# Kernel optimization log

Measured on AMD Instinct MI355X. Metric: run time of the kernel, lower is better.

Reference implementation:

```python
import jax, jax.numpy as jnp
import numpy as np

EPS = 1e-6
NUM_GROUPS = 32


def group_norm(x, w, b):
    # x: [B, C, W, H, L]
    B, C = x.shape[0], x.shape[1]
    xr = x.reshape(B, NUM_GROUPS, C // NUM_GROUPS, -1)
    mu = jnp.mean(xr, axis=(2, 3), keepdims=True)
    var = jnp.var(xr, axis=(2, 3), keepdims=True)
    xn = ((xr - mu) * jax.lax.rsqrt(var + EPS)).reshape(x.shape)
    return xn * w[None, :, None, None, None] + b[None, :, None, None, None]


def setup_inputs() -> dict:
    key = jax.random.key(0)
    ks = jax.random.split(key, 8)
    B, C, W, H, L = 2, 512, 16, 16, 16
    s = 1.0 / np.sqrt(C)
    return {
        "x": jax.random.normal(ks[0], (B, C, W, H, L), dtype=jnp.float32),
        "gn_w": jnp.ones((C,), dtype=jnp.float32),
        "gn_b": jnp.zeros((C,), dtype=jnp.float32),
        "q_w": jax.random.normal(ks[1], (C, C), dtype=jnp.float32) * s,
        "q_b": jnp.zeros((C,), dtype=jnp.float32),
        "k_w": jax.random.normal(ks[2], (C, C), dtype=jnp.float32) * s,
        "k_b": jnp.zeros((C,), dtype=jnp.float32),
        "v_w": jax.random.normal(ks[3], (C, C), dtype=jnp.float32) * s,
        "v_b": jnp.zeros((C,), dtype=jnp.float32),
        "p_w": jax.random.normal(ks[4], (C, C), dtype=jnp.float32) * s,
        "p_b": jnp.zeros((C,), dtype=jnp.float32),
    }


def reference(x, gn_w, gn_b, q_w, q_b, k_w, k_b, v_w, v_b, p_w, p_b):
    B, C, W, H, L = x.shape
    h = group_norm(x, gn_w, gn_b)
    hf = h.reshape(B, C, -1)  # [B, C, N]
    # 1x1 Conv3d == channel matmul: out[b,o,n] = sum_c w[o,c] * h[b,c,n] + b[o]
    q = jnp.einsum('oc,bcn->bon', q_w, hf) + q_b[None, :, None]
    k = jnp.einsum('oc,bcn->bon', k_w, hf) + k_b[None, :, None]
    v = jnp.einsum('oc,bcn->bon', v_w, hf) + v_b[None, :, None]
    scale = jnp.asarray(C, x.dtype) ** -0.5
    # w_[b,i,j] = sum_c q[b,c,i] * k[b,c,j]
    w_ = jnp.einsum('bci,bcj->bij', q, k) * scale
    w_ = jax.nn.softmax(w_, axis=2)
    # h_[b,c,i] = sum_j v[b,c,j] * w_[b,i,j]
    attn = jnp.einsum('bcj,bij->bci', v, w_)
    proj = jnp.einsum('oc,bcn->bon', p_w, attn) + p_b[None, :, None]
    return x + proj.reshape(B, C, W, H, L)
```

## Files before the change

### kernel.cpp

```cpp
#include <hip/hip_runtime.h>


typedef __bf16 bf16;
typedef __attribute__((ext_vector_type(8))) __bf16 bf16x8;
typedef __attribute__((ext_vector_type(4))) __bf16 bf16x4;
typedef __attribute__((ext_vector_type(4))) float f32x4;

#define CC 512
#define NN 4096
#define BM 128
#define BN 128
#define BK 64
#define SCALE_L2E 0.06376237870903338f

__device__ __forceinline__ void gload16(const bf16* g, bf16* l) {
    __builtin_amdgcn_global_load_lds(
        (const __attribute__((address_space(1))) unsigned int*)g,
        (__attribute__((address_space(3))) unsigned int*)l, 16, 0, 0);
}

__device__ __forceinline__ void gemm_core(
    const bf16* __restrict__ A, int lda,
    const bf16* __restrict__ B, int ldb,
    int kBeg, int kEnd, int m0, int n0, f32x4 acc[4][4])
{
    __shared__ __align__(16) bf16 Als[2][BM][BK];
    __shared__ __align__(16) bf16 Bls[2][BN][BK];
    const int t    = threadIdx.x;
    const int lane = t & 63;
    const int wid  = t >> 6;
    const int wm   = (wid >> 1) * 64;
    const int wn   = (wid & 1) * 64;
    const int fr   = lane & 15;
    const int kq   = lane >> 4;
    const int r_   = t >> 3;
    const int cbs  = (t & 7) ^ (r_ & 7);
    const int dcol = (t & 7) * 8;
    const int cs0  = ((kq)     ^ (fr & 7)) * 8;
    const int cs1  = ((kq + 4) ^ (fr & 7)) * 8;

    const bf16* Ab = A + (size_t)(m0 + r_) * lda + cbs * 8;
    const bf16* Bb = B + (size_t)(n0 + r_) * ldb + cbs * 8;

#define STAGE_G(bufi, kk) do {                                              \
        _Pragma("unroll")                                                   \
        for (int i = 0; i < 4; ++i)                                         \
            gload16(Ab + (kk) + (size_t)(i * 32) * lda,                     \
                    &Als[bufi][i * 32 + r_][dcol]);                         \
        _Pragma("unroll")                                                   \
        for (int i = 0; i < 4; ++i)                                         \
            gload16(Bb + (kk) + (size_t)(i * 32) * ldb,                     \
                    &Bls[bufi][i * 32 + r_][dcol]);                         \
    } while (0)

    int cur = 0;
    STAGE_G(0, kBeg);
    __syncthreads();
    for (int k0 = kBeg; k0 < kEnd; k0 += BK) {
        if (k0 + BK < kEnd) STAGE_G(cur ^ 1, k0 + BK);
        #pragma unroll
        for (int h = 0; h < 2; ++h) {
            const int cs = h ? cs1 : cs0;
            bf16x8 af[4], bg[4];
            #pragma unroll
            for (int f = 0; f < 4; ++f) {
                af[f] = *(const bf16x8*)&Als[cur][wm + f * 16 + fr][cs];
                bg[f] = *(const bf16x8*)&Bls[cur][wn + f * 16 + fr][cs];
            }
            #pragma unroll
            for (int fm = 0; fm < 4; ++fm)
                #pragma unroll
                for (int fn = 0; fn < 4; ++fn)
                    acc[fm][fn] = __builtin_amdgcn_mfma_f32_16x16x32_bf16(
                        af[fm], bg[fn], acc[fm][fn], 0, 0, 0);
        }
        __syncthreads();
        cur ^= 1;
    }
#undef STAGE_G
}

__device__ __forceinline__ void gemm_core64(
    const bf16* __restrict__ A, int lda,
    const bf16* __restrict__ B, int ldb,
    int kBeg, int kEnd, int m0, int n0, f32x4 acc[2][4])
{
    __shared__ __align__(16) bf16 Als[2][64][BK];
    __shared__ __align__(16) bf16 Bls[2][BN][BK];
    const int t    = threadIdx.x;
    const int lane = t & 63;
    const int wid  = t >> 6;
    const int wm   = (wid >> 1) * 32;
    const int wn   = (wid & 1) * 64;
    const int fr   = lane & 15;
    const int kq   = lane >> 4;
    const int r_   = t >> 3;
    const int cbs  = (t & 7) ^ (r_ & 7);
    const int dcol = (t & 7) * 8;
    const int cs0  = ((kq)     ^ (fr & 7)) * 8;
    const int cs1  = ((kq + 4) ^ (fr & 7)) * 8;

    const bf16* Ab = A + (size_t)(m0 + r_) * lda + cbs * 8;
    const bf16* Bb = B + (size_t)(n0 + r_) * ldb + cbs * 8;

#define STAGE_G64(bufi, kk) do {                                            \
        _Pragma("unroll")                                                   \
        for (int i = 0; i < 2; ++i)                                         \
            gload16(Ab + (kk) + (size_t)(i * 32) * lda,                     \
                    &Als[bufi][i * 32 + r_][dcol]);                         \
        _Pragma("unroll")                                                   \
        for (int i = 0; i < 4; ++i)                                         \
            gload16(Bb + (kk) + (size_t)(i * 32) * ldb,                     \
                    &Bls[bufi][i * 32 + r_][dcol]);                         \
    } while (0)

    int cur = 0;
    STAGE_G64(0, kBeg);
    __syncthreads();
    for (int k0 = kBeg; k0 < kEnd; k0 += BK) {
        if (k0 + BK < kEnd) STAGE_G64(cur ^ 1, k0 + BK);
        #pragma unroll
        for (int h = 0; h < 2; ++h) {
            const int cs = h ? cs1 : cs0;
            bf16x8 af[2], bg[4];
            #pragma unroll
            for (int f = 0; f < 2; ++f)
                af[f] = *(const bf16x8*)&Als[cur][wm + f * 16 + fr][cs];
            #pragma unroll
            for (int f = 0; f < 4; ++f)
                bg[f] = *(const bf16x8*)&Bls[cur][wn + f * 16 + fr][cs];
            #pragma unroll
            for (int fm = 0; fm < 2; ++fm)
                #pragma unroll
                for (int fn = 0; fn < 4; ++fn)
                    acc[fm][fn] = __builtin_amdgcn_mfma_f32_16x16x32_bf16(
                        af[fm], bg[fn], acc[fm][fn], 0, 0, 0);
        }
        __syncthreads();
        cur ^= 1;
    }
#undef STAGE_G64
}

__global__ __launch_bounds__(256) void convert_w_kernel(
    const float* __restrict__ qw, const float* __restrict__ kw,
    const float* __restrict__ pw, bf16* __restrict__ dst)
{
    const int which = blockIdx.y;
    const float* src = which == 0 ? qw : which == 1 ? kw : pw;
    const int slot  = which == 2 ? 3 : which;
    bf16* d = dst + (size_t)slot * (CC * CC);
    const int f4 = blockIdx.x * 256 + threadIdx.x;
    float4 v = ((const float4*)src)[f4];
    bf16x4 o;
    o[0] = (bf16)v.x; o[1] = (bf16)v.y; o[2] = (bf16)v.z; o[3] = (bf16)v.w;
    ((bf16x4*)d)[f4] = o;
}

__global__ __launch_bounds__(256) void vwT_kernel(
    const float* __restrict__ vw, bf16* __restrict__ vwT)
{
    const int k0 = blockIdx.x * 64;
    const int c0 = blockIdx.y * 64;
    const int t  = threadIdx.x;
    const int tk = t & 15, tc = t >> 4;
    float o[4][4];
    #pragma unroll
    for (int j = 0; j < 4; ++j) {
        const int c = c0 + tc * 4 + j;
        float4 v = *(const float4*)(vw + (size_t)c * CC + k0 + tk * 4);
        o[j][0] = v.x; o[j][1] = v.y; o[j][2] = v.z; o[j][3] = v.w;
    }
    #pragma unroll
    for (int i = 0; i < 4; ++i) {
        bf16x4 w4;
        w4[0] = (bf16)o[0][i]; w4[1] = (bf16)o[1][i];
        w4[2] = (bf16)o[2][i]; w4[3] = (bf16)o[3][i];
        *(bf16x4*)(vwT + (size_t)(k0 + tk * 4 + i) * CC + c0 + tc * 4) = w4;
    }
}

__global__ __launch_bounds__(256) void wb_kernel(
    const float* __restrict__ pw, const float* __restrict__ vb,
    float* __restrict__ wb)
{
    const int o = blockIdx.x * 256 + threadIdx.x;
    const float4* row = (const float4*)(pw + (size_t)o * CC);
    const float4* v4  = (const float4*)vb;
    float s = 0.f;
    #pragma unroll 4
    for (int i = 0; i < 128; ++i) {
        float4 a = row[i], b = v4[i];
        s += a.x * b.x + a.y * b.y + a.z * b.z + a.w * b.w;
    }
    wb[o] = s;
}

__global__ __launch_bounds__(256) void gn_stats_kernel(
    const float* __restrict__ x, float* __restrict__ mr)
{
    const int bg = blockIdx.x >> 2;
    const int qq = blockIdx.x & 3;
    const float4* base = (const float4*)(x + (size_t)bg * 16 * NN);
    const int t = threadIdx.x;
    float s = 0.f, sq = 0.f;
    #pragma unroll 4
    for (int i = 0; i < 16; ++i) {
        float4 v = base[(qq * 16 + i) * 256 + t];
        s  += v.x + v.y + v.z + v.w;
        sq += v.x * v.x + v.y * v.y + v.z * v.z + v.w * v.w;
    }
    #pragma unroll
    for (int o = 32; o > 0; o >>= 1) { s += __shfl_xor(s, o); sq += __shfl_xor(sq, o); }
    __shared__ float rs[4], rq[4];
    const int lane = t & 63, wid = t >> 6;
    if (lane == 0) { rs[wid] = s; rq[wid] = sq; }
    __syncthreads();
    if (t == 0) {
        atomicAdd(&mr[bg * 2],     rs[0] + rs[1] + rs[2] + rs[3]);
        atomicAdd(&mr[bg * 2 + 1], rq[0] + rq[1] + rq[2] + rq[3]);
    }
}

__global__ __launch_bounds__(256) void gn_apply_T_kernel(
    const float* __restrict__ x, const float* __restrict__ gw,
    const float* __restrict__ gb, const float* __restrict__ mr,
    bf16* __restrict__ hT)
{
    const int b  = blockIdx.z;
    const int n0 = blockIdx.x * 64;
    const int c0 = blockIdx.y * 64;
    const int t  = threadIdx.x;
    const int tn = t & 15, tc = t >> 4;
    float o[4][4];
    #pragma unroll
    for (int j = 0; j < 4; ++j) {
        const int c = c0 + tc * 4 + j;
        const int bg = b * 32 + (c >> 4);
        const float invn = 1.f / 65536.f;
        const float mean = mr[bg * 2] * invn;
        const float var  = mr[bg * 2 + 1] * invn - mean * mean;
        const float rstd = rsqrtf(var + 1e-6f);
        const float w  = gw[c] * rstd;
        const float bb = gb[c] - mean * w;
        float4 v = *(const float4*)(x + ((size_t)(b * CC + c)) * NN + n0 + tn * 4);
        o[j][0] = v.x * w + bb; o[j][1] = v.y * w + bb;
        o[j][2] = v.z * w + bb; o[j][3] = v.w * w + bb;
    }
    bf16* dst = hT + (size_t)b * (size_t)NN * CC;
    #pragma unroll
    for (int i = 0; i < 4; ++i) {
        bf16x4 w4;
        w4[0] = (bf16)o[0][i]; w4[1] = (bf16)o[1][i];
        w4[2] = (bf16)o[2][i]; w4[3] = (bf16)o[3][i];
        *(bf16x4*)(dst + (size_t)(n0 + tn * 4 + i) * CC + c0 + tc * 4) = w4;
    }
}

__global__ __launch_bounds__(256) void fw_gemm_kernel(
    const bf16* __restrict__ pwb, const bf16* __restrict__ vwT,
    bf16* __restrict__ fw)
{
    const int m0 = blockIdx.y * BM, n0 = blockIdx.x * BN;
    f32x4 acc[4][4] = {};
    gemm_core(pwb, CC, vwT, CC, 0, CC, m0, n0, acc);
    const int lane = threadIdx.x & 63, wid = threadIdx.x >> 6;
    const int wm = (wid >> 1) * 64, wn = (wid & 1) * 64;
    const int cf = lane & 15, rb = (lane >> 4) * 4;
    #pragma unroll
    for (int fm = 0; fm < 4; ++fm)
      #pragma unroll
      for (int fn = 0; fn < 4; ++fn)
        #pragma unroll
        for (int r = 0; r < 4; ++r)
            fw[(size_t)(m0 + wm + fm * 16 + rb + r) * CC
               + (n0 + wn + fn * 16 + cf)] = (bf16)acc[fm][fn][r];
}

__global__ __launch_bounds__(256) void qkw_gemm_kernel(
    const bf16* __restrict__ hT, const bf16* __restrict__ wbf,
    const bf16* __restrict__ fw,
    const float* __restrict__ qb, const float* __restrict__ kb,
    bf16* __restrict__ qT, bf16* __restrict__ kT, bf16* __restrict__ Wt)
{
    const size_t CN = (size_t)CC * NN;
    const int id = blockIdx.x;
    const int seg = id >> 7, s = id & 127;

    const bf16* A; const bf16* B;
    int m0, n0, ldo; bf16* outp; const float* bias; int role;
    if (seg < 4) {
        role = seg & 1;
        const int b = seg >> 1;
        A = hT + (size_t)b * CN;
        B = wbf + (size_t)role * CC * CC;
        m0 = (s >> 2) * 128; n0 = (s & 3) * 128;
        outp = (role ? kT : qT) + (size_t)b * CN; ldo = CC;
        bias = role ? kb : qb;
    } else {
        role = 2;
        const int b = seg - 4;
        A = fw;
        B = hT + (size_t)b * CN;
        m0 = (s >> 5) * 128; n0 = (s & 31) * 128;
        outp = Wt + (size_t)b * CN; ldo = NN;
        bias = nullptr;
    }
    f32x4 acc[4][4] = {};
    gemm_core(A, CC, B, CC, 0, CC, m0, n0, acc);
    const int lane = threadIdx.x & 63, wid = threadIdx.x >> 6;
    const int wm = (wid >> 1) * 64, wn = (wid & 1) * 64;
    const int cf = lane & 15, rb = (lane >> 4) * 4;
    #pragma unroll
    for (int fm = 0; fm < 4; ++fm)
      #pragma unroll
      for (int fn = 0; fn < 4; ++fn) {
          const int col = n0 + wn + fn * 16 + cf;
          const float bv = (role < 2) ? bias[col] : 0.f;
          #pragma unroll
          for (int r = 0; r < 4; ++r) {
              const int row = m0 + wm + fm * 16 + rb + r;
              float val = acc[fm][fn][r] + bv;
              if (role == 0) val *= SCALE_L2E;
              outp[(size_t)row * ldo + col] = (bf16)val;
          }
      }
}

__global__ __launch_bounds__(256) void se_gemm_kernel(
    const bf16* __restrict__ qT, const bf16* __restrict__ kT,
    bf16* __restrict__ E, float* __restrict__ rowsum)
{
    const int b = blockIdx.z;
    const size_t CN = (size_t)CC * NN;
    const bf16* qT_b = qT + (size_t)b * CN;
    const bf16* kT_b = kT + (size_t)b * CN;
    bf16* E_b = E + (size_t)b * NN * NN;
    float* rs_b = rowsum + (size_t)b * NN;
    const int m0 = blockIdx.y * BM, n0 = blockIdx.x * BN;
    f32x4 acc[4][4] = {};
    gemm_core(qT_b, CC, kT_b, CC, 0, CC, m0, n0, acc);
    const int lane = threadIdx.x & 63, wid = threadIdx.x >> 6;
    const int wm = (wid >> 1) * 64, wn = (wid & 1) * 64;
    const int cf = lane & 15, rb = (lane >> 4) * 4;
    #pragma unroll
    for (int fm = 0; fm < 4; ++fm)
      #pragma unroll
      for (int fn = 0; fn < 4; ++fn)
        #pragma unroll
        for (int r = 0; r < 4; ++r) {
            float e = exp2f(fminf(acc[fm][fn][r], 86.f));
            acc[fm][fn][r] = e;
            E_b[(size_t)(m0 + wm + fm * 16 + rb + r) * NN
                + (n0 + wn + fn * 16 + cf)] = (bf16)e;
        }
    #pragma unroll
    for (int fm = 0; fm < 4; ++fm)
      #pragma unroll
      for (int r = 0; r < 4; ++r) {
          float s = acc[fm][0][r] + acc[fm][1][r] + acc[fm][2][r] + acc[fm][3][r];
          s += __shfl_xor(s, 1); s += __shfl_xor(s, 2);
          s += __shfl_xor(s, 4); s += __shfl_xor(s, 8);
          if (cf == 0)
              atomicAdd(&rs_b[m0 + wm + fm * 16 + rb + r], s);
      }
}

__global__ __launch_bounds__(256) void pvproj_kernel(
    const bf16* __restrict__ Wt, const bf16* __restrict__ E,
    const float* __restrict__ rowsum, const float* __restrict__ wb,
    const float* __restrict__ pb, const float* __restrict__ x,
    float* __restrict__ outp)
{
    const int b = blockIdx.z;
    const size_t CN = (size_t)CC * NN;
    const int m0 = blockIdx.y * 64, n0 = blockIdx.x * BN;
    f32x4 acc[2][4] = {};
    gemm_core64(Wt + (size_t)b * CN, NN, E + (size_t)b * NN * NN, NN,
                0, NN, m0, n0, acc);
    const float* rs_b = rowsum + (size_t)b * NN;
    const int lane = threadIdx.x & 63, wid = threadIdx.x >> 6;
    const int wm = (wid >> 1) * 32, wn = (wid & 1) * 64;
    const int cf = lane & 15, rb = (lane >> 4) * 4;
    #pragma unroll
    for (int fm = 0; fm < 2; ++fm)
      #pragma unroll
      for (int g = 0; g < 4; ++g) {
          const int col = n0 + wn + g * 16 + cf;
          const float inv = 1.f / rs_b[col];
          #pragma unroll
          for (int r = 0; r < 4; ++r) {
              const int row = m0 + wm + fm * 16 + rb + r;
              const size_t idx = (size_t)b * CN + (size_t)row * NN + col;
              outp[idx] = acc[fm][g][r] * inv + wb[row] + pb[row] + x[idx];
          }
      }
}

extern "C" void kernel_launch(void* const* d_in, const int* in_sizes, int n_in,
                              void* d_out, int out_size, void* d_ws, size_t ws_size,
                              hipStream_t stream)
{
    const float* x   = (const float*)d_in[0];
    const float* gnw = (const float*)d_in[1];
    const float* gnb = (const float*)d_in[2];
    const float* qw  = (const float*)d_in[3];
    const float* qb  = (const float*)d_in[4];
    const float* kw  = (const float*)d_in[5];
    const float* kb  = (const float*)d_in[6];
    const float* vw  = (const float*)d_in[7];
    const float* vb  = (const float*)d_in[8];
    const float* pw  = (const float*)d_in[9];
    const float* pb  = (const float*)d_in[10];
    float* outp = (float*)d_out;

    char* ws = (char*)d_ws;
    size_t off = 0;
    auto alloc = [&](size_t bytes) -> char* {
        char* p = ws + off;
        off = (off + bytes + 255) & ~(size_t)255;
        return p;
    };
    const size_t CN = (size_t)CC * NN;
    bf16*  wbf  = (bf16*)alloc(4 * (size_t)CC * CC * sizeof(bf16));
    bf16*  hT   = (bf16*)alloc(2 * CN * sizeof(bf16));
    bf16*  qT   = (bf16*)alloc(2 * CN * sizeof(bf16));
    bf16*  kT   = (bf16*)alloc(2 * CN * sizeof(bf16));
    bf16*  fw   = (bf16*)alloc((size_t)CC * CC * sizeof(bf16));
    bf16*  Wt   = (bf16*)alloc(2 * CN * sizeof(bf16));
    bf16*  E    = (bf16*)alloc(2 * (size_t)NN * NN * sizeof(bf16));
    float* rowsum = (float*)alloc(2 * NN * sizeof(float));
    float* wb   = (float*)alloc(CC * sizeof(float));
    float* mr   = (float*)alloc(64 * 2 * sizeof(float));

    bf16* vwT = wbf + 2 * (size_t)CC * CC;
    bf16* pwb = wbf + 3 * (size_t)CC * CC;

    convert_w_kernel<<<dim3(256, 3), 256, 0, stream>>>(qw, kw, pw, wbf);
    vwT_kernel<<<dim3(8, 8), 256, 0, stream>>>(vw, vwT);
    wb_kernel<<<2, 256, 0, stream>>>(pw, vb, wb);
    hipMemsetAsync(mr, 0, 64 * 2 * sizeof(float), stream);
    gn_stats_kernel<<<256, 256, 0, stream>>>(x, mr);
    gn_apply_T_kernel<<<dim3(NN / 64, CC / 64, 2), 256, 0, stream>>>(
        x, gnw, gnb, mr, hT);
    hipMemsetAsync(rowsum, 0, 2 * NN * sizeof(float), stream);

    fw_gemm_kernel<<<dim3(4, 4), 256, 0, stream>>>(pwb, vwT, fw);
    qkw_gemm_kernel<<<768, 256, 0, stream>>>(
        hT, wbf, fw, qb, kb, qT, kT, Wt);

    se_gemm_kernel<<<dim3(NN / BN, NN / BM, 2), 256, 0, stream>>>(
        qT, kT, E, rowsum);

    pvproj_kernel<<<dim3(NN / BN, 8, 2), 256, 0, stream>>>(
        Wt, E, rowsum, wb, pb, x, outp);
}
```

Baseline: 206.0 us.

## Rewrite score GEMM as 256x256 tile, 8-wave, phase-pipelined kernel

```diff
diff --git a/kernel.cpp b/kernel.cpp
--- a/kernel.cpp
+++ b/kernel.cpp
@@ -1,4 +1,5 @@
 #include <hip/hip_runtime.h>
+#include <type_traits>
 
 
 typedef __bf16 bf16;
@@ -327,42 +328,136 @@
       }
 }
 
-__global__ __launch_bounds__(256) void se_gemm_kernel(
+__global__ __launch_bounds__(512) void se8_kernel(
     const bf16* __restrict__ qT, const bf16* __restrict__ kT,
     bf16* __restrict__ E, float* __restrict__ rowsum)
 {
+    __shared__ __align__(16) bf16 Als[2][256][64];
+    __shared__ __align__(16) bf16 Bls[2][256][64];
+
     const int b = blockIdx.z;
     const size_t CN = (size_t)CC * NN;
-    const bf16* qT_b = qT + (size_t)b * CN;
-    const bf16* kT_b = kT + (size_t)b * CN;
+    const bf16* A = qT + (size_t)b * CN;
+    const bf16* Bm = kT + (size_t)b * CN;
+    const int m0 = blockIdx.y * 256, n0 = blockIdx.x * 256;
+
+    const int t    = threadIdx.x;
+    const int lane = t & 63;
+    const int wid  = t >> 6;
+    const int wr   = wid >> 2;
+    const int wc   = wid & 3;
+    const int fr   = lane & 15;
+    const int kq   = lane >> 4;
+    const int cs0  = ((kq)     ^ (fr & 7)) * 8;
+    const int cs1  = ((kq + 4) ^ (fr & 7)) * 8;
+
+    const int rr0 = t >> 3;
+    const int bl0 = t & 7;
+
+    auto SB = [&](int kt, int h) {
+        #pragma unroll
+        for (int j = 0; j < 2; ++j) {
+            const int r = rr0 + j * 64 + h * 128;
+            const int src = bl0 ^ (r & 7);
+            gload16(Bm + (size_t)(n0 + r) * CC + kt * 64 + src * 8,
+                    &Bls[kt & 1][r][bl0 * 8]);
+        }
+    };
+    auto SA = [&](int kt, int s) {
+        #pragma unroll
+        for (int j = 0; j < 2; ++j) {
+            const int r = rr0 + s * 64 + j * 128;
+            const int src = bl0 ^ (r & 7);
+            gload16(A + (size_t)(m0 + r) * CC + kt * 64 + src * 8,
+                    &Als[kt & 1][r][bl0 * 8]);
+        }
+    };
+
+    f32x4 acc[8][4] = {};
+    bf16x8 bf_[4][2];
+
+    auto phase = [&](int kt, auto qc, auto stage, int waitmode) {
+        constexpr int Q = decltype(qc)::value;
+        const int db = kt & 1;
+        if (Q == 0) {
+            #pragma unroll
+            for (int g = 0; g < 4; ++g) {
+                const int br = wc * 64 + g * 16 + fr;
+                bf_[g][0] = *(const bf16x8*)&Bls[db][br][cs0];
+                bf_[g][1] = *(const bf16x8*)&Bls[db][br][cs1];
+            }
+        }
+        bf16x8 af_[2][2];
+        #pragma unroll
+        for (int f = 0; f < 2; ++f) {
+            const int ar = wr * 128 + Q * 32 + f * 16 + fr;
+            af_[f][0] = *(const bf16x8*)&Als[db][ar][cs0];
+            af_[f][1] = *(const bf16x8*)&Als[db][ar][cs1];
+        }
+        stage();
+        if (waitmode == 1)      asm volatile("s_waitcnt vmcnt(6)" ::: "memory");
+        else if (waitmode == 2) asm volatile("s_waitcnt vmcnt(0)" ::: "memory");
+        __builtin_amdgcn_s_barrier();
+        asm volatile("s_waitcnt lgkmcnt(0)" ::: "memory");
+        __builtin_amdgcn_sched_barrier(0);
+        __builtin_amdgcn_s_setprio(1);
+        #pragma unroll
+        for (int kh = 0; kh < 2; ++kh)
+            #pragma unroll
+            for (int f = 0; f < 2; ++f)
+                #pragma unroll
+                for (int g = 0; g < 4; ++g)
+                    acc[Q * 2 + f][g] = __builtin_amdgcn_mfma_f32_16x16x32_bf16(
+                        af_[f][kh], bf_[g][kh], acc[Q * 2 + f][g], 0, 0, 0);
+        __builtin_amdgcn_s_setprio(0);
+        __builtin_amdgcn_s_barrier();
+    };
+
+    SB(0, 0); SB(0, 1); SA(0, 0); SA(0, 1);
+    SB(1, 0); SB(1, 1); SA(1, 0);
+    asm volatile("s_waitcnt vmcnt(6)" ::: "memory");
+    __builtin_amdgcn_s_barrier();
+
+    #define IC(v) std::integral_constant<int, v>{}
+    for (int i = 0; i < 4; ++i) {
+        const int k0t = 2 * i, k1t = 2 * i + 1;
+        const int T2 = 2 * i + 2, T3 = 2 * i + 3;
+        const bool more = (i < 3);
+        const int wm_ = more ? 1 : 2;
+        phase(k0t, IC(0), [&]{ SA(k1t, 1); },            0);
+        phase(k0t, IC(1), [&]{ if (more) SB(T2, 0); },   0);
+        phase(k0t, IC(2), [&]{ if (more) SB(T2, 1); },   0);
+        phase(k0t, IC(3), [&]{ if (more) SA(T2, 0); },   wm_);
+        phase(k1t, IC(0), [&]{ if (more) SA(T2, 1); },   0);
+        phase(k1t, IC(1), [&]{ if (more) SB(T3, 0); },   0);
+        phase(k1t, IC(2), [&]{ if (more) SB(T3, 1); },   0);
+        phase(k1t, IC(3), [&]{ if (more) SA(T3, 0); },   wm_);
+    }
+    #undef IC
+
     bf16* E_b = E + (size_t)b * NN * NN;
     float* rs_b = rowsum + (size_t)b * NN;
-    const int m0 = blockIdx.y * BM, n0 = blockIdx.x * BN;
-    f32x4 acc[4][4] = {};
-    gemm_core(qT_b, CC, kT_b, CC, 0, CC, m0, n0, acc);
-    const int lane = threadIdx.x & 63, wid = threadIdx.x >> 6;
-    const int wm = (wid >> 1) * 64, wn = (wid & 1) * 64;
-    const int cf = lane & 15, rb = (lane >> 4) * 4;
-    #pragma unroll
-    for (int fm = 0; fm < 4; ++fm)
+    const int cf = fr, rb = kq * 4;
+    #pragma unroll
+    for (int fm = 0; fm < 8; ++fm)
       #pragma unroll
-      for (int fn = 0; fn < 4; ++fn)
+      for (int g = 0; g < 4; ++g)
         #pragma unroll
         for (int r = 0; r < 4; ++r) {
-            float e = exp2f(fminf(acc[fm][fn][r], 86.f));
-            acc[fm][fn][r] = e;
-            E_b[(size_t)(m0 + wm + fm * 16 + rb + r) * NN
-                + (n0 + wn + fn * 16 + cf)] = (bf16)e;
-        }
-    #pragma unroll
-    for (int fm = 0; fm < 4; ++fm)
+            float e = exp2f(fminf(acc[fm][g][r], 86.f));
+            acc[fm][g][r] = e;
+            E_b[(size_t)(m0 + wr * 128 + fm * 16 + rb + r) * NN
+                + (n0 + wc * 64 + g * 16 + cf)] = (bf16)e;
+        }
+    #pragma unroll
+    for (int fm = 0; fm < 8; ++fm)
       #pragma unroll
       for (int r = 0; r < 4; ++r) {
           float s = acc[fm][0][r] + acc[fm][1][r] + acc[fm][2][r] + acc[fm][3][r];
           s += __shfl_xor(s, 1); s += __shfl_xor(s, 2);
           s += __shfl_xor(s, 4); s += __shfl_xor(s, 8);
           if (cf == 0)
-              atomicAdd(&rs_b[m0 + wm + fm * 16 + rb + r], s);
+              atomicAdd(&rs_b[m0 + wr * 128 + fm * 16 + rb + r], s);
       }
 }
 
@@ -449,8 +544,7 @@
     qkw_gemm_kernel<<<768, 256, 0, stream>>>(
         hT, wbf, fw, qb, kb, qT, kT, Wt);
 
-    se_gemm_kernel<<<dim3(NN / BN, NN / BM, 2), 256, 0, stream>>>(
-        qT, kT, E, rowsum);
+    se8_kernel<<<dim3(16, 16, 2), 512, 0, stream>>>(qT, kT, E, rowsum);
 
     pvproj_kernel<<<dim3(NN / BN, 8, 2), 256, 0, stream>>>(
         Wt, E, rowsum, wb, pb, x, outp);
```

Measured after the change: 202.2 us, median of 2. Within noise of the previous version (-1.8%).

## Replace double-buffered LDS staging with single-buffer load-sync-compute loop

Applied to the files above, without the earlier changes.

```diff
diff --git a/kernel.cpp b/kernel.cpp
--- a/kernel.cpp
+++ b/kernel.cpp
@@ -19,13 +19,13 @@
         (__attribute__((address_space(3))) unsigned int*)l, 16, 0, 0);
 }
 
-__device__ __forceinline__ void gemm_core(
+__device__ __forceinline__ void gemm_core_sb(
     const bf16* __restrict__ A, int lda,
     const bf16* __restrict__ B, int ldb,
     int kBeg, int kEnd, int m0, int n0, f32x4 acc[4][4])
 {
-    __shared__ __align__(16) bf16 Als[2][BM][BK];
-    __shared__ __align__(16) bf16 Bls[2][BN][BK];
+    __shared__ __align__(16) bf16 Als[BM][BK];
+    __shared__ __align__(16) bf16 Bls[BN][BK];
     const int t    = threadIdx.x;
     const int lane = t & 63;
     const int wid  = t >> 6;
@@ -42,30 +42,22 @@
     const bf16* Ab = A + (size_t)(m0 + r_) * lda + cbs * 8;
     const bf16* Bb = B + (size_t)(n0 + r_) * ldb + cbs * 8;
 
-#define STAGE_G(bufi, kk) do {                                              \
-        _Pragma("unroll")                                                   \
-        for (int i = 0; i < 4; ++i)                                         \
-            gload16(Ab + (kk) + (size_t)(i * 32) * lda,                     \
-                    &Als[bufi][i * 32 + r_][dcol]);                         \
-        _Pragma("unroll")                                                   \
-        for (int i = 0; i < 4; ++i)                                         \
-            gload16(Bb + (kk) + (size_t)(i * 32) * ldb,                     \
-                    &Bls[bufi][i * 32 + r_][dcol]);                         \
-    } while (0)
-
-    int cur = 0;
-    STAGE_G(0, kBeg);
-    __syncthreads();
     for (int k0 = kBeg; k0 < kEnd; k0 += BK) {
-        if (k0 + BK < kEnd) STAGE_G(cur ^ 1, k0 + BK);
+        #pragma unroll
+        for (int i = 0; i < 4; ++i)
+            gload16(Ab + k0 + (size_t)(i * 32) * lda, &Als[i * 32 + r_][dcol]);
+        #pragma unroll
+        for (int i = 0; i < 4; ++i)
+            gload16(Bb + k0 + (size_t)(i * 32) * ldb, &Bls[i * 32 + r_][dcol]);
+        __syncthreads();
         #pragma unroll
         for (int h = 0; h < 2; ++h) {
             const int cs = h ? cs1 : cs0;
             bf16x8 af[4], bg[4];
             #pragma unroll
             for (int f = 0; f < 4; ++f) {
-                af[f] = *(const bf16x8*)&Als[cur][wm + f * 16 + fr][cs];
-                bg[f] = *(const bf16x8*)&Bls[cur][wn + f * 16 + fr][cs];
+                af[f] = *(const bf16x8*)&Als[wm + f * 16 + fr][cs];
+                bg[f] = *(const bf16x8*)&Bls[wn + f * 16 + fr][cs];
             }
             #pragma unroll
             for (int fm = 0; fm < 4; ++fm)
@@ -75,9 +67,7 @@
                         af[fm], bg[fn], acc[fm][fn], 0, 0, 0);
         }
         __syncthreads();
-        cur ^= 1;
-    }
-#undef STAGE_G
+    }
 }
 
 __device__ __forceinline__ void gemm_core64(
@@ -263,7 +253,7 @@
 {
     const int m0 = blockIdx.y * BM, n0 = blockIdx.x * BN;
     f32x4 acc[4][4] = {};
-    gemm_core(pwb, CC, vwT, CC, 0, CC, m0, n0, acc);
+    gemm_core_sb(pwb, CC, vwT, CC, 0, CC, m0, n0, acc);
     const int lane = threadIdx.x & 63, wid = threadIdx.x >> 6;
     const int wm = (wid >> 1) * 64, wn = (wid & 1) * 64;
     const int cf = lane & 15, rb = (lane >> 4) * 4;
@@ -307,7 +297,7 @@
         bias = nullptr;
     }
     f32x4 acc[4][4] = {};
-    gemm_core(A, CC, B, CC, 0, CC, m0, n0, acc);
+    gemm_core_sb(A, CC, B, CC, 0, CC, m0, n0, acc);
     const int lane = threadIdx.x & 63, wid = threadIdx.x >> 6;
     const int wm = (wid >> 1) * 64, wn = (wid & 1) * 64;
     const int cf = lane & 15, rb = (lane >> 4) * 4;
@@ -339,7 +329,7 @@
     float* rs_b = rowsum + (size_t)b * NN;
     const int m0 = blockIdx.y * BM, n0 = blockIdx.x * BN;
     f32x4 acc[4][4] = {};
-    gemm_core(qT_b, CC, kT_b, CC, 0, CC, m0, n0, acc);
+    gemm_core_sb(qT_b, CC, kT_b, CC, 0, CC, m0, n0, acc);
     const int lane = threadIdx.x & 63, wid = threadIdx.x >> 6;
     const int wm = (wid >> 1) * 64, wn = (wid & 1) * 64;
     const int cf = lane & 15, rb = (lane >> 4) * 4;
```

New measurement: 206.5 us. Within noise of the previous version (+0.2%).
